# Optimization experiments

Measured on AMD Instinct MI355X. Metric: run time of the kernel, lower is better.

The kernel has to match this reference:

```python
import jax, jax.numpy as jnp
import numpy as np

D = 128      # entity_and_theorem_embedding_size
M = 8192     # nodes per tree level
L = 5        # internal (non-leaf) levels
V = 4096     # number of input entities (leaf vocab)
K = 8        # number of binary numerical functions
KL = 4       # number of binary logic functions
G = 4096     # number of ground-truth logic statements


def setup_inputs() -> dict:
    key = jax.random.key(0)
    ks = jax.random.split(key, 16)
    s = 0.05
    return {
        "leaf_ids": jax.random.randint(ks[0], (M,), 0, V, dtype=jnp.int32),
        "left_idx": jax.random.randint(ks[1], (L, M), 0, M, dtype=jnp.int32),
        "right_idx": jax.random.randint(ks[2], (L, M), 0, M, dtype=jnp.int32),
        "nf_fid": jax.random.randint(ks[3], (L, M), 0, K, dtype=jnp.int32),
        "gt_left": jax.random.randint(ks[4], (G,), 0, M, dtype=jnp.int32),
        "gt_right": jax.random.randint(ks[5], (G,), 0, M, dtype=jnp.int32),
        "lf_fid": jax.random.randint(ks[6], (G,), 0, KL, dtype=jnp.int32),
        "emb": jax.random.normal(ks[7], (V, D), jnp.float32),
        "W1": jax.random.normal(ks[8], (K, 2 * D, 4 * D), jnp.float32) * s,
        "b1": jnp.zeros((K, 4 * D), jnp.float32),
        "W2": jax.random.normal(ks[9], (K, 4 * D, 2 * D), jnp.float32) * s,
        "b2": jnp.zeros((K, 2 * D), jnp.float32),
        "W3": jax.random.normal(ks[10], (K, 2 * D, D), jnp.float32) * s,
        "b3": jnp.zeros((K, D), jnp.float32),
        "Wl1": jax.random.normal(ks[11], (KL, 2 * D, 4 * D), jnp.float32) * s,
        "bl1": jnp.zeros((KL, 4 * D), jnp.float32),
        "Wl2": jax.random.normal(ks[12], (KL, 4 * D, D), jnp.float32) * s,
        "bl2": jnp.zeros((KL, D), jnp.float32),
    }


def _select(y, fid):
    # y: [N, K, F], fid: [N] -> [N, F]  (per-node dynamic MLP dispatch)
    return jnp.take_along_axis(y, fid[:, None, None], axis=1)[:, 0, :]


def reference(leaf_ids, left_idx, right_idx, nf_fid, gt_left, gt_right, lf_fid,
              emb, W1, b1, W2, b2, W3, b3, Wl1, bl1, Wl2, bl2):
    # Leaf entities: embedding lookup (input_entity_embedding)
    h0 = emb[leaf_ids]  # [M, D]

    # Internal entity nodes: recursive nf_two2one MLPs, level-synchronous
    def level(h, xs):
        li, ri, fid = xs
        x = jnp.concatenate([h[li], h[ri]], axis=-1)          # [M, 2D] concat of operands
        a1 = jax.nn.relu(jnp.einsum('nd,kdf->nkf', x, W1) + b1)   # [M, K, 4D]
        a2 = jax.nn.relu(jnp.einsum('nkd,kdf->nkf', a1, W2) + b2) # [M, K, 2D]
        a3 = jnp.einsum('nkd,kdf->nkf', a2, W3) + b3              # [M, K, D]
        return _select(a3, fid), None
    hL, _ = jax.lax.scan(level, h0, (left_idx, right_idx, nf_fid))

    # Logic statements: lf_two2one MLP on pairs of entity encodings
    xg = jnp.concatenate([hL[gt_left], hL[gt_right]], axis=-1)    # [G, 2D]
    g1 = jax.nn.relu(jnp.einsum('nd,kdf->nkf', xg, Wl1) + bl1)    # [G, KL, 4D]
    g2 = jnp.einsum('nkd,kdf->nkf', g1, Wl2) + bl2                # [G, KL, D]
    return _select(g2, lf_fid)                                    # [G, D]
```

## Files before the change

kernel.cpp:

```cpp
#include <hip/hip_runtime.h>

constexpr int D  = 128;
constexpr int M  = 8192;
constexpr int L  = 5;
constexpr int K  = 8;
constexpr int KL = 4;
constexpr int G  = 4096;

constexpr int TB   = 64;
constexpr int PADL = M + K * TB;
constexpr int PADG = G + KL * TB;

typedef short bf16x8 __attribute__((ext_vector_type(8)));
typedef float f32x4  __attribute__((ext_vector_type(4)));

__device__ __forceinline__ unsigned short f2bf(float x) {
  union { float f; unsigned int u; } c; c.f = x;
  unsigned int u = c.u + 0x7FFF + ((c.u >> 16) & 1);
  return (unsigned short)(u >> 16);
}
__device__ __forceinline__ float bf2f(unsigned short h) {
  union { unsigned int u; float f; } c; c.u = ((unsigned int)h) << 16;
  return c.f;
}

__global__ void leaf_gather_kernel(const int* __restrict__ leaf_ids,
                                   const float* __restrict__ emb,
                                   float* __restrict__ h0) {
  int idx = blockIdx.x * 256 + threadIdx.x;
  int n = idx >> 7, d = idx & 127;
  h0[idx] = emb[(size_t)leaf_ids[n] * D + d];
}

__global__ void bucket64_kernel(const int* __restrict__ nf_fid,
                                const int* __restrict__ lf_fid,
                                int* __restrict__ orders) {
  int b = blockIdx.x;
  const int* fid; int N, Kf, cap; int* out;
  if (b < L) { fid = nf_fid + b * M; N = M; Kf = K;  cap = PADL; out = orders + b * PADL; }
  else       { fid = lf_fid;         N = G; Kf = KL; cap = PADG; out = orders + L * PADL; }
  __shared__ int cnt[8];
  __shared__ int cur[8];
  int tid = threadIdx.x;
  if (tid < Kf) cnt[tid] = 0;
  __syncthreads();
  for (int i = tid; i < N; i += 256) atomicAdd(&cnt[fid[i]], 1);
  __syncthreads();
  if (tid == 0) {
    int off = 0;
    for (int k = 0; k < Kf; ++k) { cur[k] = off; off += ((cnt[k] + TB - 1) / TB) * TB; }
  }
  __syncthreads();
  for (int i = tid; i < cap; i += 256) out[i] = -1;
  __syncthreads();
  for (int i = tid; i < N; i += 256) {
    int kk = fid[i];
    int pos = atomicAdd(&cur[kk], 1);
    out[pos] = i;
  }
}

__global__ void prep_kernel(const float* __restrict__ W1, const float* __restrict__ W2,
                            const float* __restrict__ W3, const float* __restrict__ Wl1,
                            const float* __restrict__ Wl2,
                            short* __restrict__ B1T, short* __restrict__ B2T,
                            short* __restrict__ B3T, short* __restrict__ BL1T,
                            short* __restrict__ BL2T) {
  int b = blockIdx.x;
  const float* W; short* BT; int KD, F;
  if      (b < 4096) { W = W1;  BT = B1T;  KD = 256; F = 512; }
  else if (b < 6144) { W = W2;  BT = B2T;  KD = 512; F = 256; b -= 4096; }
  else if (b < 7168) { W = W3;  BT = B3T;  KD = 256; F = 128; b -= 6144; }
  else if (b < 9216) { W = Wl1; BT = BL1T; KD = 256; F = 512; b -= 7168; }
  else               { W = Wl2; BT = BL2T; KD = 512; F = 128; b -= 9216; }
  int k = b / F, f = b % F;
  for (int d = threadIdx.x; d < KD; d += 256) {
    float w = W[((size_t)k * KD + d) * F + f];
    unsigned short hi = f2bf(w);
    unsigned short lo = f2bf(w - bf2f(hi));
    BT[((size_t)k * F + f) * (2 * KD) + d]      = (short)hi;
    BT[((size_t)k * F + f) * (2 * KD) + KD + d] = (short)lo;
  }
}

template<int KH, int NN, int EPI, int FUSED, int TROWS>
__global__ __launch_bounds__(256) void mfma_gemm(
    const short* __restrict__ A, const float* __restrict__ hsrc,
    const int* __restrict__ gl, const int* __restrict__ gr,
    const short* __restrict__ BT, const float* __restrict__ bias,
    short* __restrict__ Aout, float* __restrict__ outp,
    const int* __restrict__ order, const int* __restrict__ fid) {
  static_assert(FUSED == 0 || TROWS == 64, "fused gather assumes 64-row tiles");
  constexpr int BK  = 64;
  constexpr int NCH = 3 * KH / BK;
  constexpr int LDA = BK + 8;
  constexpr int RF  = TROWS / 32;
  constexpr int TPR = 256 / TROWS;
  __shared__ __align__(16) short As[TROWS * LDA];
  __shared__ __align__(16) short Bs[128 * LDA];
  __shared__ int nodesS[TROWS], liS[TROWS], riS[TROWS];

  const int tid = threadIdx.x;
  const int row0 = blockIdx.x * TROWS;
  const int ct = blockIdx.y;

  if (tid < TROWS) {
    int node = order[row0 + tid];
    nodesS[tid] = node;
    if (FUSED) {
      liS[tid] = node >= 0 ? gl[node] : 0;
      riS[tid] = node >= 0 ? gr[node] : 0;
    }
  }
  __syncthreads();
  if (nodesS[0] < 0) return;
  const int kfn = fid[nodesS[0]];
  const short* __restrict__ Bk = BT + (size_t)kfn * NN * (2 * KH);

  const int lane = tid & 63, wave = tid >> 6;
  const int wr = (wave >> 1) * (TROWS / 2);
  const int wc = wave & 1;
  const int l15 = lane & 15, oct = lane >> 4;

  const int ar = tid / TPR;
  const int ag = (tid % TPR) * (BK / TPR);
  const int bn = tid >> 1;
  const int bg = (tid & 1) * 32;

  f32x4 acc[RF][4];
  #pragma unroll
  for (int i = 0; i < RF; ++i)
    #pragma unroll
    for (int j = 0; j < 4; ++j) acc[i][j] = (f32x4)0.f;

  int4 A00, A01, A10, A11;
  float4 F00, F01, F02, F03, F10, F11, F12, F13;
  int4 B00, B01, B02, B03, B10, B11, B12, B13;

  auto loadB_to = [&](int c, int4& r0, int4& r1, int4& r2, int4& r3) {
    int ko = c * BK, seg = ko / KH, wi = ko % KH;
    int pb = (seg == 2) ? KH + wi : wi;
    const int4* p = (const int4*)(Bk + (size_t)(ct * 128 + bn) * (2 * KH) + pb + bg);
    r0 = p[0]; r1 = p[1]; r2 = p[2]; r3 = p[3];
  };
  auto loadA_to = [&](int c, int4& r0, int4& r1,
                      float4& f0, float4& f1, float4& f2, float4& f3) {
    int ko = c * BK, seg = ko / KH, wi = ko % KH;
    if (FUSED) {
      int dl = wi + ag;
      if (nodesS[ar] >= 0) {
        const float* src = (dl < 128) ? (hsrc + (size_t)liS[ar] * 128 + dl)
                                      : (hsrc + (size_t)riS[ar] * 128 + (dl - 128));
        const float4* p = (const float4*)src;
        f0 = p[0]; f1 = p[1]; f2 = p[2]; f3 = p[3];
      } else {
        f0 = f1 = f2 = f3 = make_float4(0.f, 0.f, 0.f, 0.f);
      }
    } else {
      int pa = (seg == 1) ? KH + wi : wi;
      const int4* p = (const int4*)(A + (size_t)(row0 + ar) * (2 * KH) + pa + ag);
      r0 = p[0];
      if (TPR == 4) r1 = p[1];
    }
  };
  auto storeLDS_from = [&](int c, int4& r0, int4& r1,
                           float4& f0, float4& f1, float4& f2, float4& f3,
                           int4& b0, int4& b1, int4& b2, int4& b3) {
    if (FUSED) {
      int seg = (c * BK) / KH;
      float v[16];
      ((float4*)v)[0] = f0; ((float4*)v)[1] = f1;
      ((float4*)v)[2] = f2; ((float4*)v)[3] = f3;
      union { unsigned short u[16]; int4 q[2]; } o;
      if (seg != 1) {
        #pragma unroll
        for (int i = 0; i < 16; ++i) o.u[i] = f2bf(v[i]);
      } else {
        #pragma unroll
        for (int i = 0; i < 16; ++i) {
          unsigned short hh = f2bf(v[i]);
          o.u[i] = f2bf(v[i] - bf2f(hh));
        }
      }
      int4* d4 = (int4*)&As[ar * LDA + ag];
      d4[0] = o.q[0]; d4[1] = o.q[1];
    } else {
      int4* d4 = (int4*)&As[ar * LDA + ag];
      d4[0] = r0;
      if (TPR == 4) d4[1] = r1;
    }
    int4* db = (int4*)&Bs[bn * LDA + bg];
    db[0] = b0; db[1] = b1; db[2] = b2; db[3] = b3;
  };
  auto compute = [&]() {
    #pragma unroll
    for (int s = 0; s < 2; ++s) {
      const int ko = s * 32 + oct * 8;
      bf16x8 afr[RF];
      #pragma unroll
      for (int rf = 0; rf < RF; ++rf)
        afr[rf] = *(const bf16x8*)&As[(wr + rf * 16 + l15) * LDA + ko];
      #pragma unroll
      for (int cf = 0; cf < 4; ++cf) {
        bf16x8 b = *(const bf16x8*)&Bs[(wc * 64 + cf * 16 + l15) * LDA + ko];
        #pragma unroll
        for (int rf = 0; rf < RF; ++rf)
          acc[rf][cf] = __builtin_amdgcn_mfma_f32_16x16x32_bf16(afr[rf], b, acc[rf][cf], 0, 0, 0);
      }
    }
  };

  loadA_to(0, A00, A01, F00, F01, F02, F03);
  loadB_to(0, B00, B01, B02, B03);
  loadA_to(1, A10, A11, F10, F11, F12, F13);
  loadB_to(1, B10, B11, B12, B13);
  for (int c = 0; c < NCH; c += 2) {
    __syncthreads();
    storeLDS_from(c, A00, A01, F00, F01, F02, F03, B00, B01, B02, B03);
    __syncthreads();
    if (c + 2 < NCH) {
      loadA_to(c + 2, A00, A01, F00, F01, F02, F03);
      loadB_to(c + 2, B00, B01, B02, B03);
    }
    compute();
    __syncthreads();
    storeLDS_from(c + 1, A10, A11, F10, F11, F12, F13, B10, B11, B12, B13);
    __syncthreads();
    if (c + 3 < NCH) {
      loadA_to(c + 3, A10, A11, F10, F11, F12, F13);
      loadB_to(c + 3, B10, B11, B12, B13);
    }
    compute();
  }

  if (EPI == 0) {
    short* Ls = (short*)Bs;
    #pragma unroll
    for (int part = 0; part < 2; ++part) {
      __syncthreads();
      #pragma unroll
      for (int rf = 0; rf < RF; ++rf)
        #pragma unroll
        for (int cf = 0; cf < 4; ++cf) {
          int colL = wc * 64 + cf * 16 + l15;
          float bv = bias[kfn * NN + ct * 128 + colL];
          #pragma unroll
          for (int j = 0; j < 4; ++j) {
            int row = wr + rf * 16 + oct * 4 + j;
            float v = fmaxf(acc[rf][cf][j] + bv, 0.f);
            unsigned short hh = f2bf(v);
            unsigned short val = (part == 0) ? hh : f2bf(v - bf2f(hh));
            Ls[row * 128 + colL] = (short)val;
          }
        }
      __syncthreads();
      constexpr int SPT = TROWS / 2;
      constexpr int TPW = 128 / SPT;
      int row = tid / TPW, sg = (tid % TPW) * SPT;
      const int4* src = (const int4*)&Ls[row * 128 + sg];
      int4* dst = (int4*)&Aout[(size_t)(row0 + row) * (2 * NN) + part * NN + ct * 128 + sg];
      #pragma unroll
      for (int q = 0; q < SPT / 8; ++q) dst[q] = src[q];
    }
  } else {
    float* Lf = (float*)Bs;
    #pragma unroll
    for (int h = 0; h < 2; ++h) {
      __syncthreads();
      if (wc == h) {
        #pragma unroll
        for (int rf = 0; rf < RF; ++rf)
          #pragma unroll
          for (int cf = 0; cf < 4; ++cf) {
            int colL = cf * 16 + l15;
            float bv = bias[kfn * 128 + h * 64 + colL];
            #pragma unroll
            for (int j = 0; j < 4; ++j) {
              int row = wr + rf * 16 + oct * 4 + j;
              Lf[row * 64 + colL] = acc[rf][cf][j] + bv;
            }
          }
      }
      __syncthreads();
      constexpr int FPT = TROWS / 4;
      constexpr int TPW = 64 / FPT;
      int row = tid / TPW, off = (tid % TPW) * FPT;
      int node = nodesS[row];
      if (node >= 0) {
        const float4* src = (const float4*)&Lf[row * 64 + off];
        float4* dst = (float4*)&outp[(size_t)node * 128 + h * 64 + off];
        #pragma unroll
        for (int q = 0; q < FPT / 4; ++q) dst[q] = src[q];
      }
    }
  }
}

extern "C" void kernel_launch(void* const* d_in, const int* in_sizes, int n_in,
                              void* d_out, int out_size, void* d_ws, size_t ws_size,
                              hipStream_t stream) {
  const int*   leaf_ids  = (const int*)d_in[0];
  const int*   left_idx  = (const int*)d_in[1];
  const int*   right_idx = (const int*)d_in[2];
  const int*   nf_fid    = (const int*)d_in[3];
  const int*   gt_left   = (const int*)d_in[4];
  const int*   gt_right  = (const int*)d_in[5];
  const int*   lf_fid    = (const int*)d_in[6];
  const float* emb       = (const float*)d_in[7];
  const float* W1 = (const float*)d_in[8];
  const float* b1 = (const float*)d_in[9];
  const float* W2 = (const float*)d_in[10];
  const float* b2 = (const float*)d_in[11];
  const float* W3 = (const float*)d_in[12];
  const float* b3 = (const float*)d_in[13];
  const float* Wl1 = (const float*)d_in[14];
  const float* bl1 = (const float*)d_in[15];
  const float* Wl2 = (const float*)d_in[16];
  const float* bl2 = (const float*)d_in[17];
  float* out = (float*)d_out;

  const size_t SZ_H    = (size_t)M * D * 4;
  const size_t SZ_A1   = (size_t)PADL * 1024 * 2;
  const size_t SZ_A2   = (size_t)PADL * 512 * 2;
  const size_t SZ_B1T  = (size_t)8 * 512 * 512 * 2;
  const size_t SZ_B2T  = (size_t)8 * 256 * 1024 * 2;
  const size_t SZ_B3T  = (size_t)8 * 128 * 512 * 2;
  const size_t SZ_BL1T = (size_t)4 * 512 * 512 * 2;
  const size_t SZ_BL2T = (size_t)4 * 128 * 1024 * 2;

  char* p = (char*)d_ws;
  float* hA   = (float*)p;  p += SZ_H;
  float* hB   = (float*)p;  p += SZ_H;
  short* a1s  = (short*)p;  p += SZ_A1;
  short* a2s  = (short*)p;  p += SZ_A2;
  short* B1T  = (short*)p;  p += SZ_B1T;
  short* B2T  = (short*)p;  p += SZ_B2T;
  short* B3T  = (short*)p;  p += SZ_B3T;
  short* BL1T = (short*)p;  p += SZ_BL1T;
  short* BL2T = (short*)p;  p += SZ_BL2T;
  int*   orders = (int*)p;

  leaf_gather_kernel<<<(M * D) / 256, 256, 0, stream>>>(leaf_ids, emb, hA);
  bucket64_kernel<<<L + 1, 256, 0, stream>>>(nf_fid, lf_fid, orders);
  prep_kernel<<<9728, 256, 0, stream>>>(W1, W2, W3, Wl1, Wl2,
                                        B1T, B2T, B3T, BL1T, BL2T);

  float* hin = hA;
  float* hout = hB;
  for (int l = 0; l < L; ++l) {
    const int* ord = orders + l * PADL;
    const int* fidl = nf_fid + l * M;
    mfma_gemm<256, 512, 0, 1, 64><<<dim3(PADL / 64, 4), 256, 0, stream>>>(
        nullptr, hin, left_idx + l * M, right_idx + l * M,
        B1T, b1, a1s, nullptr, ord, fidl);
    mfma_gemm<512, 256, 0, 0, 64><<<dim3(PADL / 64, 2), 256, 0, stream>>>(
        a1s, nullptr, nullptr, nullptr,
        B2T, b2, a2s, nullptr, ord, fidl);
    mfma_gemm<256, 128, 1, 0, 32><<<dim3(PADL / 32, 1), 256, 0, stream>>>(
        a2s, nullptr, nullptr, nullptr,
        B3T, b3, nullptr, hout, ord, fidl);
    float* t = hin; hin = hout; hout = t;
  }
  const int* ordG = orders + L * PADL;
  mfma_gemm<256, 512, 0, 1, 64><<<dim3(PADG / 64, 4), 256, 0, stream>>>(
      nullptr, hin, gt_left, gt_right,
      BL1T, bl1, a1s, nullptr, ordG, lf_fid);
  mfma_gemm<512, 128, 1, 0, 32><<<dim3(PADG / 32, 1), 256, 0, stream>>>(
      a1s, nullptr, nullptr, nullptr,
      BL2T, bl2, nullptr, out, ordG, lf_fid);
}
```

Baseline: 511.5 us.

## Store hidden states as split bf16, double-buffer LDS, and shrink row tiles to 32

Hidden states are now kept as pre-split hi/lo bf16 pairs, written by the leaf gather and by a new epilogue on the third GEMM. The fused-gather GEMM therefore loads ready bf16 data instead of converting fp32 on every tile. The GEMM main loop switches to double-buffered LDS with one barrier per chunk and raises MFMA priority with setprio. All GEMMs use 32-row tiles with occupancy hint 3, which gives more blocks but less B reuse per block.

```diff
diff --git a/kernel.cpp b/kernel.cpp
--- a/kernel.cpp
+++ b/kernel.cpp
@@ -26,10 +26,13 @@
 
 __global__ void leaf_gather_kernel(const int* __restrict__ leaf_ids,
                                    const float* __restrict__ emb,
-                                   float* __restrict__ h0) {
+                                   short* __restrict__ hs) {
   int idx = blockIdx.x * 256 + threadIdx.x;
   int n = idx >> 7, d = idx & 127;
-  h0[idx] = emb[(size_t)leaf_ids[n] * D + d];
+  float w = emb[(size_t)leaf_ids[n] * D + d];
+  unsigned short hh = f2bf(w);
+  hs[n * 256 + d]       = (short)hh;
+  hs[n * 256 + 128 + d] = (short)f2bf(w - bf2f(hh));
 }
 
 __global__ void bucket64_kernel(const int* __restrict__ nf_fid,
@@ -83,26 +86,24 @@
   }
 }
 
-template<int KH, int NN, int EPI, int FUSED, int TROWS>
-__global__ __launch_bounds__(256) void mfma_gemm(
-    const short* __restrict__ A, const float* __restrict__ hsrc,
+template<int KH, int NN, int EPI, int FUSED>
+__global__ __launch_bounds__(256, 3) void mfma_gemm(
+    const short* __restrict__ A, const short* __restrict__ hsrc,
     const int* __restrict__ gl, const int* __restrict__ gr,
     const short* __restrict__ BT, const float* __restrict__ bias,
     short* __restrict__ Aout, float* __restrict__ outp,
     const int* __restrict__ order, const int* __restrict__ fid) {
-  static_assert(FUSED == 0 || TROWS == 64, "fused gather assumes 64-row tiles");
-  constexpr int BK  = 64;
-  constexpr int NCH = 3 * KH / BK;
-  constexpr int LDA = BK + 8;
-  constexpr int RF  = TROWS / 32;
-  constexpr int TPR = 256 / TROWS;
-  __shared__ __align__(16) short As[TROWS * LDA];
-  __shared__ __align__(16) short Bs[128 * LDA];
+  constexpr int BK    = 64;
+  constexpr int NCH   = 3 * KH / BK;
+  constexpr int LDA   = BK + 8;
+  constexpr int TROWS = 32;
+  __shared__ __align__(16) short As[2][TROWS * LDA];
+  __shared__ __align__(16) short Bs[2][128 * LDA];
   __shared__ int nodesS[TROWS], liS[TROWS], riS[TROWS];
 
-  const int tid = threadIdx.x;
+  const int tid  = threadIdx.x;
   const int row0 = blockIdx.x * TROWS;
-  const int ct = blockIdx.y;
+  const int ct   = blockIdx.y;
 
   if (tid < TROWS) {
     int node = order[row0 + tid];
@@ -118,24 +119,18 @@
   const short* __restrict__ Bk = BT + (size_t)kfn * NN * (2 * KH);
 
   const int lane = tid & 63, wave = tid >> 6;
-  const int wr = (wave >> 1) * (TROWS / 2);
+  const int wr = (wave >> 1) * 16;
   const int wc = wave & 1;
   const int l15 = lane & 15, oct = lane >> 4;
 
-  const int ar = tid / TPR;
-  const int ag = (tid % TPR) * (BK / TPR);
+  const int ar = tid >> 3;
+  const int ag = (tid & 7) * 8;
   const int bn = tid >> 1;
   const int bg = (tid & 1) * 32;
 
-  f32x4 acc[RF][4];
+  f32x4 acc[4];
   #pragma unroll
-  for (int i = 0; i < RF; ++i)
-    #pragma unroll
-    for (int j = 0; j < 4; ++j) acc[i][j] = (f32x4)0.f;
-
-  int4 A00, A01, A10, A11;
-  float4 F00, F01, F02, F03, F10, F11, F12, F13;
-  int4 B00, B01, B02, B03, B10, B11, B12, B13;
+  for (int j = 0; j < 4; ++j) acc[j] = (f32x4)0.f;
 
   auto loadB_to = [&](int c, int4& r0, int4& r1, int4& r2, int4& r3) {
     int ko = c * BK, seg = ko / KH, wi = ko % KH;
@@ -143,155 +138,131 @@
     const int4* p = (const int4*)(Bk + (size_t)(ct * 128 + bn) * (2 * KH) + pb + bg);
     r0 = p[0]; r1 = p[1]; r2 = p[2]; r3 = p[3];
   };
-  auto loadA_to = [&](int c, int4& r0, int4& r1,
-                      float4& f0, float4& f1, float4& f2, float4& f3) {
+  auto loadA_to = [&](int c, int4& r0) {
     int ko = c * BK, seg = ko / KH, wi = ko % KH;
+    int pa = ((seg == 1) ? KH : 0) + wi + ag;
     if (FUSED) {
-      int dl = wi + ag;
+      int s4 = pa >> 7;
+      int node = (s4 & 1) ? riS[ar] : liS[ar];
       if (nodesS[ar] >= 0) {
-        const float* src = (dl < 128) ? (hsrc + (size_t)liS[ar] * 128 + dl)
-                                      : (hsrc + (size_t)riS[ar] * 128 + (dl - 128));
-        const float4* p = (const float4*)src;
-        f0 = p[0]; f1 = p[1]; f2 = p[2]; f3 = p[3];
+        r0 = *(const int4*)(hsrc + (size_t)node * 256 + ((s4 >> 1) << 7) + (pa & 127));
       } else {
-        f0 = f1 = f2 = f3 = make_float4(0.f, 0.f, 0.f, 0.f);
+        r0 = make_int4(0, 0, 0, 0);
       }
     } else {
-      int pa = (seg == 1) ? KH + wi : wi;
-      const int4* p = (const int4*)(A + (size_t)(row0 + ar) * (2 * KH) + pa + ag);
-      r0 = p[0];
-      if (TPR == 4) r1 = p[1];
-    }
-  };
-  auto storeLDS_from = [&](int c, int4& r0, int4& r1,
-                           float4& f0, float4& f1, float4& f2, float4& f3,
-                           int4& b0, int4& b1, int4& b2, int4& b3) {
-    if (FUSED) {
-      int seg = (c * BK) / KH;
-      float v[16];
-      ((float4*)v)[0] = f0; ((float4*)v)[1] = f1;
-      ((float4*)v)[2] = f2; ((float4*)v)[3] = f3;
-      union { unsigned short u[16]; int4 q[2]; } o;
-      if (seg != 1) {
-        #pragma unroll
-        for (int i = 0; i < 16; ++i) o.u[i] = f2bf(v[i]);
-      } else {
-        #pragma unroll
-        for (int i = 0; i < 16; ++i) {
-          unsigned short hh = f2bf(v[i]);
-          o.u[i] = f2bf(v[i] - bf2f(hh));
-        }
-      }
-      int4* d4 = (int4*)&As[ar * LDA + ag];
-      d4[0] = o.q[0]; d4[1] = o.q[1];
-    } else {
-      int4* d4 = (int4*)&As[ar * LDA + ag];
-      d4[0] = r0;
-      if (TPR == 4) d4[1] = r1;
-    }
-    int4* db = (int4*)&Bs[bn * LDA + bg];
-    db[0] = b0; db[1] = b1; db[2] = b2; db[3] = b3;
-  };
-  auto compute = [&]() {
+      r0 = *(const int4*)(A + (size_t)(row0 + ar) * (2 * KH) + pa);
+    }
+  };
+  auto storeA = [&](int b, const int4& r0) {
+    *(int4*)&As[b][ar * LDA + ag] = r0;
+  };
+  auto storeB = [&](int b, const int4& r0, const int4& r1, const int4& r2, const int4& r3) {
+    int4* db = (int4*)&Bs[b][bn * LDA + bg];
+    db[0] = r0; db[1] = r1; db[2] = r2; db[3] = r3;
+  };
+  auto compute = [&](int b) {
+    __builtin_amdgcn_s_setprio(1);
     #pragma unroll
     for (int s = 0; s < 2; ++s) {
       const int ko = s * 32 + oct * 8;
-      bf16x8 afr[RF];
-      #pragma unroll
-      for (int rf = 0; rf < RF; ++rf)
-        afr[rf] = *(const bf16x8*)&As[(wr + rf * 16 + l15) * LDA + ko];
+      bf16x8 afr = *(const bf16x8*)&As[b][(wr + l15) * LDA + ko];
       #pragma unroll
       for (int cf = 0; cf < 4; ++cf) {
-        bf16x8 b = *(const bf16x8*)&Bs[(wc * 64 + cf * 16 + l15) * LDA + ko];
-        #pragma unroll
-        for (int rf = 0; rf < RF; ++rf)
-          acc[rf][cf] = __builtin_amdgcn_mfma_f32_16x16x32_bf16(afr[rf], b, acc[rf][cf], 0, 0, 0);
-      }
-    }
-  };
-
-  loadA_to(0, A00, A01, F00, F01, F02, F03);
-  loadB_to(0, B00, B01, B02, B03);
-  loadA_to(1, A10, A11, F10, F11, F12, F13);
-  loadB_to(1, B10, B11, B12, B13);
+        bf16x8 bb = *(const bf16x8*)&Bs[b][(wc * 64 + cf * 16 + l15) * LDA + ko];
+        acc[cf] = __builtin_amdgcn_mfma_f32_16x16x32_bf16(afr, bb, acc[cf], 0, 0, 0);
+      }
+    }
+    __builtin_amdgcn_s_setprio(0);
+  };
+
+  int4 a0, a1, b00, b01, b02, b03, b10, b11, b12, b13;
+  loadA_to(0, a0); loadB_to(0, b00, b01, b02, b03);
+  loadA_to(1, a1); loadB_to(1, b10, b11, b12, b13);
+  storeA(0, a0); storeB(0, b00, b01, b02, b03);
+  __syncthreads();
   for (int c = 0; c < NCH; c += 2) {
+    storeA(1, a1); storeB(1, b10, b11, b12, b13);
+    if (c + 2 < NCH) { loadA_to(c + 2, a0); loadB_to(c + 2, b00, b01, b02, b03); }
+    compute(0);
     __syncthreads();
-    storeLDS_from(c, A00, A01, F00, F01, F02, F03, B00, B01, B02, B03);
+    if (c + 2 < NCH) { storeA(0, a0); storeB(0, b00, b01, b02, b03); }
+    if (c + 3 < NCH) { loadA_to(c + 3, a1); loadB_to(c + 3, b10, b11, b12, b13); }
+    compute(1);
     __syncthreads();
-    if (c + 2 < NCH) {
-      loadA_to(c + 2, A00, A01, F00, F01, F02, F03);
-      loadB_to(c + 2, B00, B01, B02, B03);
-    }
-    compute();
-    __syncthreads();
-    storeLDS_from(c + 1, A10, A11, F10, F11, F12, F13, B10, B11, B12, B13);
-    __syncthreads();
-    if (c + 3 < NCH) {
-      loadA_to(c + 3, A10, A11, F10, F11, F12, F13);
-      loadB_to(c + 3, B10, B11, B12, B13);
-    }
-    compute();
   }
 
   if (EPI == 0) {
-    short* Ls = (short*)Bs;
+    short* Ls = (short*)&Bs[0][0];
     #pragma unroll
     for (int part = 0; part < 2; ++part) {
       __syncthreads();
       #pragma unroll
-      for (int rf = 0; rf < RF; ++rf)
+      for (int cf = 0; cf < 4; ++cf) {
+        int colL = wc * 64 + cf * 16 + l15;
+        float bv = bias[kfn * NN + ct * 128 + colL];
         #pragma unroll
-        for (int cf = 0; cf < 4; ++cf) {
-          int colL = wc * 64 + cf * 16 + l15;
-          float bv = bias[kfn * NN + ct * 128 + colL];
-          #pragma unroll
-          for (int j = 0; j < 4; ++j) {
-            int row = wr + rf * 16 + oct * 4 + j;
-            float v = fmaxf(acc[rf][cf][j] + bv, 0.f);
-            unsigned short hh = f2bf(v);
-            unsigned short val = (part == 0) ? hh : f2bf(v - bf2f(hh));
-            Ls[row * 128 + colL] = (short)val;
-          }
+        for (int j = 0; j < 4; ++j) {
+          int row = wr + oct * 4 + j;
+          float v = fmaxf(acc[cf][j] + bv, 0.f);
+          unsigned short hh = f2bf(v);
+          unsigned short val = (part == 0) ? hh : f2bf(v - bf2f(hh));
+          Ls[row * 128 + colL] = (short)val;
         }
+      }
       __syncthreads();
-      constexpr int SPT = TROWS / 2;
-      constexpr int TPW = 128 / SPT;
-      int row = tid / TPW, sg = (tid % TPW) * SPT;
+      int row = tid >> 3, sg = (tid & 7) * 16;
       const int4* src = (const int4*)&Ls[row * 128 + sg];
       int4* dst = (int4*)&Aout[(size_t)(row0 + row) * (2 * NN) + part * NN + ct * 128 + sg];
-      #pragma unroll
-      for (int q = 0; q < SPT / 8; ++q) dst[q] = src[q];
-    }
-  } else {
-    float* Lf = (float*)Bs;
+      dst[0] = src[0]; dst[1] = src[1];
+    }
+  } else if (EPI == 1) {
+    float* Lf = (float*)&Bs[0][0];
     #pragma unroll
     for (int h = 0; h < 2; ++h) {
       __syncthreads();
       if (wc == h) {
         #pragma unroll
-        for (int rf = 0; rf < RF; ++rf)
+        for (int cf = 0; cf < 4; ++cf) {
+          int colL = cf * 16 + l15;
+          float bv = bias[kfn * 128 + h * 64 + colL];
           #pragma unroll
-          for (int cf = 0; cf < 4; ++cf) {
-            int colL = cf * 16 + l15;
-            float bv = bias[kfn * 128 + h * 64 + colL];
-            #pragma unroll
-            for (int j = 0; j < 4; ++j) {
-              int row = wr + rf * 16 + oct * 4 + j;
-              Lf[row * 64 + colL] = acc[rf][cf][j] + bv;
-            }
+          for (int j = 0; j < 4; ++j) {
+            int row = wr + oct * 4 + j;
+            Lf[row * 64 + colL] = acc[cf][j] + bv;
           }
+        }
       }
       __syncthreads();
-      constexpr int FPT = TROWS / 4;
-      constexpr int TPW = 64 / FPT;
-      int row = tid / TPW, off = (tid % TPW) * FPT;
+      int row = tid >> 3, off = (tid & 7) * 8;
       int node = nodesS[row];
       if (node >= 0) {
         const float4* src = (const float4*)&Lf[row * 64 + off];
         float4* dst = (float4*)&outp[(size_t)node * 128 + h * 64 + off];
-        #pragma unroll
-        for (int q = 0; q < FPT / 4; ++q) dst[q] = src[q];
-      }
+        dst[0] = src[0]; dst[1] = src[1];
+      }
+    }
+  } else {
+    short* Ls = (short*)&Bs[0][0];
+    #pragma unroll
+    for (int cf = 0; cf < 4; ++cf) {
+      int colL = wc * 64 + cf * 16 + l15;
+      float bv = bias[kfn * 128 + colL];
+      #pragma unroll
+      for (int j = 0; j < 4; ++j) {
+        int row = wr + oct * 4 + j;
+        float v = acc[cf][j] + bv;
+        unsigned short hh = f2bf(v);
+        Ls[row * 256 + colL]       = (short)hh;
+        Ls[row * 256 + 128 + colL] = (short)f2bf(v - bf2f(hh));
+      }
+    }
+    __syncthreads();
+    int row = tid >> 3, sg = (tid & 7) * 32;
+    int node = nodesS[row];
+    if (node >= 0) {
+      const int4* src = (const int4*)&Ls[row * 256 + sg];
+      int4* dst = (int4*)&Aout[(size_t)node * 256 + sg];
+      dst[0] = src[0]; dst[1] = src[1]; dst[2] = src[2]; dst[3] = src[3];
     }
   }
 }
@@ -319,7 +290,7 @@
   const float* bl2 = (const float*)d_in[17];
   float* out = (float*)d_out;
 
-  const size_t SZ_H    = (size_t)M * D * 4;
+  const size_t SZ_H    = (size_t)M * 256 * 2;
   const size_t SZ_A1   = (size_t)PADL * 1024 * 2;
   const size_t SZ_A2   = (size_t)PADL * 512 * 2;
   const size_t SZ_B1T  = (size_t)8 * 512 * 512 * 2;
@@ -329,8 +300,8 @@
   const size_t SZ_BL2T = (size_t)4 * 128 * 1024 * 2;
 
   char* p = (char*)d_ws;
-  float* hA   = (float*)p;  p += SZ_H;
-  float* hB   = (float*)p;  p += SZ_H;
+  short* hsA  = (short*)p;  p += SZ_H;
+  short* hsB  = (short*)p;  p += SZ_H;
   short* a1s  = (short*)p;  p += SZ_A1;
   short* a2s  = (short*)p;  p += SZ_A2;
   short* B1T  = (short*)p;  p += SZ_B1T;
@@ -340,32 +311,32 @@
   short* BL2T = (short*)p;  p += SZ_BL2T;
   int*   orders = (int*)p;
 
-  leaf_gather_kernel<<<(M * D) / 256, 256, 0, stream>>>(leaf_ids, emb, hA);
+  leaf_gather_kernel<<<(M * D) / 256, 256, 0, stream>>>(leaf_ids, emb, hsA);
   bucket64_kernel<<<L + 1, 256, 0, stream>>>(nf_fid, lf_fid, orders);
   prep_kernel<<<9728, 256, 0, stream>>>(W1, W2, W3, Wl1, Wl2,
                                         B1T, B2T, B3T, BL1T, BL2T);
 
-  float* hin = hA;
-  float* hout = hB;
+  short* hin = hsA;
+  short* hout = hsB;
   for (int l = 0; l < L; ++l) {
     const int* ord = orders + l * PADL;
     const int* fidl = nf_fid + l * M;
-    mfma_gemm<256, 512, 0, 1, 64><<<dim3(PADL / 64, 4), 256, 0, stream>>>(
+    mfma_gemm<256, 512, 0, 1><<<dim3(PADL / 32, 4), 256, 0, stream>>>(
         nullptr, hin, left_idx + l * M, right_idx + l * M,
         B1T, b1, a1s, nullptr, ord, fidl);
-    mfma_gemm<512, 256, 0, 0, 64><<<dim3(PADL / 64, 2), 256, 0, stream>>>(
+    mfma_gemm<512, 256, 0, 0><<<dim3(PADL / 32, 2), 256, 0, stream>>>(
         a1s, nullptr, nullptr, nullptr,
         B2T, b2, a2s, nullptr, ord, fidl);
-    mfma_gemm<256, 128, 1, 0, 32><<<dim3(PADL / 32, 1), 256, 0, stream>>>(
+    mfma_gemm<256, 128, 2, 0><<<dim3(PADL / 32, 1), 256, 0, stream>>>(
         a2s, nullptr, nullptr, nullptr,
-        B3T, b3, nullptr, hout, ord, fidl);
-    float* t = hin; hin = hout; hout = t;
+        B3T, b3, hout, nullptr, ord, fidl);
+    short* t = hin; hin = hout; hout = t;
   }
   const int* ordG = orders + L * PADL;
-  mfma_gemm<256, 512, 0, 1, 64><<<dim3(PADG / 64, 4), 256, 0, stream>>>(
+  mfma_gemm<256, 512, 0, 1><<<dim3(PADG / 32, 4), 256, 0, stream>>>(
       nullptr, hin, gt_left, gt_right,
       BL1T, bl1, a1s, nullptr, ordG, lf_fid);
-  mfma_gemm<512, 128, 1, 0, 32><<<dim3(PADG / 32, 1), 256, 0, stream>>>(
+  mfma_gemm<512, 128, 1, 0><<<dim3(PADG / 32, 1), 256, 0, stream>>>(
       a1s, nullptr, nullptr, nullptr,
       BL2T, bl2, nullptr, out, ordG, lf_fid);
 }
```

Result: faster. 462.7 us (-9.5%).
